# Kernel tuning notes

Measured on AMD Instinct MI355X. Metric: run time of the kernel, lower is better.

## Reference

```python
import jax, jax.numpy as jnp
import numpy as np

B = 2_000_000
L = 64
STEPS = 10
LAT_CONST = 5 * 0.03 / 200 + 0.06  # queue*lat/bw + 0.06
GRAD_CONST = 1.0 / 0.06
SEND_CONST = 2.0 / 3.0


def setup_inputs() -> dict:
    key = jax.random.key(0)
    ks = jax.random.split(key, 5)
    x = jax.random.normal(ks[0], (B, 7), dtype=jnp.float32)
    # column 0 is the loop counter i; program assumes it starts at 0 -> 10 iterations
    x = x.at[:, 0].set(0.0)
    W1 = jax.random.normal(ks[1], (3, L), dtype=jnp.float32) * 0.1
    b1 = jnp.zeros((L,), dtype=jnp.float32)
    W2 = jax.random.normal(ks[2], (L, L), dtype=jnp.float32) * 0.1
    b2 = jnp.zeros((L,), dtype=jnp.float32)
    W3 = jax.random.normal(ks[3], (L, 1), dtype=jnp.float32) * 0.1
    b3 = jnp.zeros((1,), dtype=jnp.float32)
    return {"x": x, "W1": W1, "b1": b1, "W2": W2, "b2": b2, "W3": W3, "b3": b3}


def _mlp(feat, W1, b1, W2, b2, W3, b3):
    h = jax.nn.relu(feat @ W1 + b1)
    h = jax.nn.relu(h @ W2 + b2)
    return jax.nn.sigmoid(h @ W3 + b3)[:, 0]


def reference(x, W1, b1, W2, b2, W3, b3):
    def step(state, _):
        x2 = state[:, 2]
        x6 = state[:, 6]
        # IfElse on column 6 vs comparison_bar=0.0:
        #   body  (x6 <= 0): x2 * (x6 + 1)          (assign_upper_sender_ratio)
        #   else  (x6 >  0): x2 * ((1 - x6) / 1)    (assign_down_sender_ratio, sub_l = left-sub)
        x2 = jnp.where(x6 <= 0.0, x2 * (x6 + 1.0), x2 * (1.0 - x6))
        x4 = x2 + LAT_CONST            # latency_ratio
        x5 = x2 * SEND_CONST           # sending_ratio
        x3 = x4 * GRAD_CONST           # latency_gradient
        feat = jnp.stack([x3, x4, x5], axis=1)  # [B,3]
        a = _mlp(feat, W1, b1, W2, b2, W3, b3)  # new action -> column 2
        new_state = state.at[:, 0].add(1.0)
        new_state = new_state.at[:, 2].set(a)
        new_state = new_state.at[:, 3].set(x3)
        new_state = new_state.at[:, 4].set(x4)
        new_state = new_state.at[:, 5].set(x5)
        return new_state, None

    final, _ = jax.lax.scan(step, x, None, length=STEPS)
    return final
```

## Files before the change

### kernel.cpp

```cpp
#include <hip/hip_runtime.h>
#include <math.h>

#define LAT_CONST  ((float)(5.0 * 0.03 / 200.0 + 0.06))
#define GRAD_CONST ((float)(1.0 / 0.06))
#define SEND_CONST ((float)(2.0 / 3.0))

#define NW   2048
#define LOW_ (-24.f)
#define HIW_ (24.f)
#define HW_  ((HIW_ - LOW_) / (float)NW)
#define IHW_ ((float)NW / (HIW_ - LOW_))
#define CW_  (-LOW_ * IHW_)
#define N2   2048
#define LO2  (-6.25f)
#define HI2  (1.25f)
#define H2   ((HI2 - LO2) / (float)N2)
#define IH2  ((float)N2 / (HI2 - LO2))
#define C2   (-LO2 * IH2)

#define GSZ   2080
#define GPCK  2064

__global__ __launch_bounds__(256)
void build_table_kernel(const float* __restrict__ W1, const float* __restrict__ b1,
                        const float* __restrict__ W2, const float* __restrict__ b2,
                        const float* __restrict__ W3, const float* __restrict__ b3,
                        float* __restrict__ g1, float* __restrict__ g2)
{
    __shared__ float pl[4][64];

    const int lane = threadIdx.x & 63;
    const int w    = threadIdx.x >> 6;
    const int i    = blockIdx.x * 64 + lane;

    float t;
    if (i < GSZ) t = LOW_ + (float)i * HW_;
    else         t = LO2 + (float)(i - GSZ) * H2;

    float x4 = t + LAT_CONST;
    float x5 = t * SEND_CONST;
    float x3 = x4 * GRAD_CONST;

    float h1v[64];
#pragma unroll
    for (int j = 0; j < 64; ++j) {
        float acc = b1[j];
        acc = fmaf(x3, W1[j],       acc);
        acc = fmaf(x4, W1[64 + j],  acc);
        acc = fmaf(x5, W1[128 + j], acc);
        h1v[j] = fmaxf(acc, 0.f);
    }

    const int j0 = w * 16;
    float acc[16];
#pragma unroll
    for (int u = 0; u < 16; ++u) acc[u] = b2[j0 + u];
#pragma unroll
    for (int k = 0; k < 64; ++k) {
        const float* __restrict__ w2r = W2 + k * 64 + j0;
#pragma unroll
        for (int u = 0; u < 16; ++u)
            acc[u] = fmaf(h1v[k], w2r[u], acc[u]);
    }
    float partial = 0.f;
#pragma unroll
    for (int u = 0; u < 16; ++u)
        partial = fmaf(fmaxf(acc[u], 0.f), W3[j0 + u], partial);

    pl[w][lane] = partial;
    __syncthreads();

    if (w == 0) {
        float logit = b3[0] + ((pl[0][lane] + pl[1][lane]) + (pl[2][lane] + pl[3][lane]));
        float g = 1.f / (1.f + expf(-logit));
        if (i < GSZ) g1[i] = g;
        else         g2[i - GSZ] = g;
    }
}

#define CHUNK 256
#define BLOCK 256
#define MAXGRID 1280

typedef unsigned int u32;
typedef __attribute__((address_space(3))) u32 lds_u32_t;
typedef __attribute__((address_space(1))) const u32 glb_u32_t;

__device__ __forceinline__ void gload16(const void* g, void* l) {
    __builtin_amdgcn_global_load_lds((glb_u32_t*)g, (lds_u32_t*)l, 16, 0, 0);
}

__device__ __forceinline__ u32 bfpack(float a, float b) {
    u32 ua = __float_as_uint(a), ub = __float_as_uint(b);
    ua = (ua + 0x7fffu + ((ua >> 16) & 1u)) >> 16;
    ub = (ub + 0x7fffu + ((ub >> 16) & 1u)) & 0xffff0000u;
    return (ua & 0xffffu) | ub;
}

__device__ __forceinline__ float lerp_pk(u32 u, float fr) {
    float e0 = __uint_as_float(u << 16);
    float e1 = __uint_as_float(u & 0xffff0000u);
    return fmaf(e1 - e0, fr, e0);
}

__global__ __launch_bounds__(BLOCK)
void rows_kernel(const float* __restrict__ x, const float* __restrict__ g1,
                 const float* __restrict__ g2, float* __restrict__ out,
                 int B, int nChunks)
{
    __shared__ u32 tw[GPCK];
    __shared__ u32 tn[GPCK];
    __shared__ __align__(16) float buf[2][CHUNK * 7];

    const int tid = threadIdx.x;
    const int c0  = blockIdx.x;

    {
        int rows0 = min(CHUNK, B - c0 * CHUNK);
        int nf40  = (rows0 * 7) >> 2;
        const float4* src = (const float4*)(x + (size_t)c0 * CHUNK * 7);
        for (int i = tid; i < nf40; i += BLOCK)
            gload16(src + i, &buf[0][i * 4]);
    }
    for (int i = tid; i < GPCK / 4; i += BLOCK) {
        float4 v = ((const float4*)g1)[i];
        float nx = g1[i * 4 + 4];
        tw[i*4+0] = bfpack(v.x, v.y); tw[i*4+1] = bfpack(v.y, v.z);
        tw[i*4+2] = bfpack(v.z, v.w); tw[i*4+3] = bfpack(v.w, nx);
        float4 q = ((const float4*)g2)[i];
        float ny = g2[i * 4 + 4];
        tn[i*4+0] = bfpack(q.x, q.y); tn[i*4+1] = bfpack(q.y, q.z);
        tn[i*4+2] = bfpack(q.z, q.w); tn[i*4+3] = bfpack(q.w, ny);
    }
    __syncthreads();

    int cur = 0;
    for (int c = c0; c < nChunks; c += gridDim.x) {
        int cn = c + gridDim.x;
        if (cn < nChunks) {
            int rowsN = min(CHUNK, B - cn * CHUNK);
            int nf4N  = (rowsN * 7) >> 2;
            const float4* src = (const float4*)(x + (size_t)cn * CHUNK * 7);
            for (int i = tid; i < nf4N; i += BLOCK)
                gload16(src + i, &buf[cur ^ 1][i * 4]);
        }

        int rows = min(CHUNK, B - c * CHUNK);
        float* bfr = buf[cur];
        for (int r = tid; r < rows; r += BLOCK) {
            float* row = bfr + r * 7;
            float x0 = row[0], x2 = row[2], x6 = row[6];
            float f = (x6 <= 0.f) ? (x6 + 1.f) : (1.f - x6);
            {
                float p = fmaf(x2, f * IHW_, CW_);
                p = fminf(fmaxf(p, 0.f), (float)NW);
                int idx = (int)p; float fr = p - (float)idx;
                x2 = lerp_pk(tw[idx], fr);
            }
            float af2 = f * IH2;
#pragma unroll
            for (int s = 0; s < 8; ++s) {
                float p = fmaf(x2, af2, C2);
                p = fminf(fmaxf(p, 0.f), (float)N2);
                int idx = (int)p; float fr = p - (float)idx;
                x2 = lerp_pk(tn[idx], fr);
            }
            float t = x2 * f;
            float p = fmaf(t, IH2, C2);
            p = fminf(fmaxf(p, 0.f), (float)N2);
            int idx = (int)p; float fr = p - (float)idx;
            float x2f = lerp_pk(tn[idx], fr);
            float x4 = t + LAT_CONST;
            row[0] = x0 + 10.f;
            row[2] = x2f;
            row[3] = x4 * GRAD_CONST;
            row[4] = x4;
            row[5] = t * SEND_CONST;
        }
        __syncthreads();

        {
            int nf4 = (rows * 7) >> 2;
            float4* dst = (float4*)(out + (size_t)c * CHUNK * 7);
            const float4* s4 = (const float4*)bfr;
            for (int i = tid; i < nf4; i += BLOCK) dst[i] = s4[i];
        }
        __syncthreads();
        cur ^= 1;
    }
}

static inline size_t align16h(size_t v) { return (v + 15) & ~(size_t)15; }

extern "C" void kernel_launch(void* const* d_in, const int* in_sizes, int n_in,
                              void* d_out, int out_size, void* d_ws, size_t ws_size,
                              hipStream_t stream)
{
    const float* x  = (const float*)d_in[0];
    const float* W1 = (const float*)d_in[1];
    const float* b1 = (const float*)d_in[2];
    const float* W2 = (const float*)d_in[3];
    const float* b2 = (const float*)d_in[4];
    const float* W3 = (const float*)d_in[5];
    const float* b3 = (const float*)d_in[6];
    float* out = (float*)d_out;

    int B = in_sizes[0] / 7;

    char* ws = (char*)d_ws;
    float* g1 = (float*)ws;
    float* g2 = (float*)(ws + align16h((size_t)GSZ * 4));

    int nChunks = (B + CHUNK - 1) / CHUNK;
    int grid    = (nChunks < MAXGRID) ? nChunks : MAXGRID;

    hipLaunchKernelGGL(build_table_kernel, dim3((2 * GSZ) / 64), dim3(256), 0, stream,
                       W1, b1, W2, b2, W3, b3, g1, g2);
    hipLaunchKernelGGL(rows_kernel, dim3(grid), dim3(BLOCK), 0, stream,
                       x, g1, g2, out, B, nChunks);
}
```

Before: 39.19 us.

## Drop first-step LDS table, use contiguous chunk ranges per block, raise grid

Removes the first-step bf16 table from LDS and reads that one lookup directly from global g1 in fp32. This halves per-block table LDS so more blocks fit per CU, and the grid cap rises from 1280 to 1792. Each block now handles a contiguous range of chunks instead of a grid stride, and tail handling for row counts not divisible by 4 floats is added. The cost is one scattered global gather per row for the first lookup.

```diff
diff --git a/kernel.cpp b/kernel.cpp
--- a/kernel.cpp
+++ b/kernel.cpp
@@ -80,7 +80,7 @@
 
 #define CHUNK 256
 #define BLOCK 256
-#define MAXGRID 1280
+#define MAXBLK 1792
 
 typedef unsigned int u32;
 typedef __attribute__((address_space(3))) u32 lds_u32_t;
@@ -88,6 +88,9 @@
 
 __device__ __forceinline__ void gload16(const void* g, void* l) {
     __builtin_amdgcn_global_load_lds((glb_u32_t*)g, (lds_u32_t*)l, 16, 0, 0);
+}
+__device__ __forceinline__ void gload4(const void* g, void* l) {
+    __builtin_amdgcn_global_load_lds((glb_u32_t*)g, (lds_u32_t*)l, 4, 0, 0);
 }
 
 __device__ __forceinline__ u32 bfpack(float a, float b) {
@@ -106,27 +109,27 @@
 __global__ __launch_bounds__(BLOCK)
 void rows_kernel(const float* __restrict__ x, const float* __restrict__ g1,
                  const float* __restrict__ g2, float* __restrict__ out,
-                 int B, int nChunks)
+                 int B, int nChunks, int grid)
 {
-    __shared__ u32 tw[GPCK];
     __shared__ u32 tn[GPCK];
     __shared__ __align__(16) float buf[2][CHUNK * 7];
 
     const int tid = threadIdx.x;
-    const int c0  = blockIdx.x;
+    const long long b = blockIdx.x;
+    const int cb = (int)(b * (long long)nChunks / grid);
+    const int ce = (int)((b + 1) * (long long)nChunks / grid);
 
     {
-        int rows0 = min(CHUNK, B - c0 * CHUNK);
-        int nf40  = (rows0 * 7) >> 2;
-        const float4* src = (const float4*)(x + (size_t)c0 * CHUNK * 7);
+        int rows0 = min(CHUNK, B - cb * CHUNK);
+        int nfl0  = rows0 * 7;
+        int nf40  = nfl0 >> 2;
+        const float* src = x + (size_t)cb * CHUNK * 7;
         for (int i = tid; i < nf40; i += BLOCK)
-            gload16(src + i, &buf[0][i * 4]);
+            gload16((const float4*)src + i, &buf[0][i * 4]);
+        for (int i = (nf40 << 2) + tid; i < nfl0; i += BLOCK)
+            gload4(src + i, &buf[0][i]);
     }
     for (int i = tid; i < GPCK / 4; i += BLOCK) {
-        float4 v = ((const float4*)g1)[i];
-        float nx = g1[i * 4 + 4];
-        tw[i*4+0] = bfpack(v.x, v.y); tw[i*4+1] = bfpack(v.y, v.z);
-        tw[i*4+2] = bfpack(v.z, v.w); tw[i*4+3] = bfpack(v.w, nx);
         float4 q = ((const float4*)g2)[i];
         float ny = g2[i * 4 + 4];
         tn[i*4+0] = bfpack(q.x, q.y); tn[i*4+1] = bfpack(q.y, q.z);
@@ -135,14 +138,16 @@
     __syncthreads();
 
     int cur = 0;
-    for (int c = c0; c < nChunks; c += gridDim.x) {
-        int cn = c + gridDim.x;
-        if (cn < nChunks) {
-            int rowsN = min(CHUNK, B - cn * CHUNK);
-            int nf4N  = (rowsN * 7) >> 2;
-            const float4* src = (const float4*)(x + (size_t)cn * CHUNK * 7);
+    for (int c = cb; c < ce; ++c) {
+        if (c + 1 < ce) {
+            int rowsN = min(CHUNK, B - (c + 1) * CHUNK);
+            int nflN  = rowsN * 7;
+            int nf4N  = nflN >> 2;
+            const float* src = x + (size_t)(c + 1) * CHUNK * 7;
             for (int i = tid; i < nf4N; i += BLOCK)
-                gload16(src + i, &buf[cur ^ 1][i * 4]);
+                gload16((const float4*)src + i, &buf[cur ^ 1][i * 4]);
+            for (int i = (nf4N << 2) + tid; i < nflN; i += BLOCK)
+                gload4(src + i, &buf[cur ^ 1][i]);
         }
 
         int rows = min(CHUNK, B - c * CHUNK);
@@ -155,7 +160,8 @@
                 float p = fmaf(x2, f * IHW_, CW_);
                 p = fminf(fmaxf(p, 0.f), (float)NW);
                 int idx = (int)p; float fr = p - (float)idx;
-                x2 = lerp_pk(tw[idx], fr);
+                float e0 = g1[idx], e1 = g1[idx + 1];
+                x2 = fmaf(e1 - e0, fr, e0);
             }
             float af2 = f * IH2;
 #pragma unroll
@@ -180,10 +186,12 @@
         __syncthreads();
 
         {
-            int nf4 = (rows * 7) >> 2;
-            float4* dst = (float4*)(out + (size_t)c * CHUNK * 7);
+            int nfl = rows * 7;
+            int nf4 = nfl >> 2;
+            float* dst = out + (size_t)c * CHUNK * 7;
             const float4* s4 = (const float4*)bfr;
-            for (int i = tid; i < nf4; i += BLOCK) dst[i] = s4[i];
+            for (int i = tid; i < nf4; i += BLOCK) ((float4*)dst)[i] = s4[i];
+            for (int i = (nf4 << 2) + tid; i < nfl; i += BLOCK) dst[i] = bfr[i];
         }
         __syncthreads();
         cur ^= 1;
@@ -212,10 +220,10 @@
     float* g2 = (float*)(ws + align16h((size_t)GSZ * 4));
 
     int nChunks = (B + CHUNK - 1) / CHUNK;
-    int grid    = (nChunks < MAXGRID) ? nChunks : MAXGRID;
+    int grid    = (nChunks < MAXBLK) ? nChunks : MAXBLK;
 
     hipLaunchKernelGGL(build_table_kernel, dim3((2 * GSZ) / 64), dim3(256), 0, stream,
                        W1, b1, W2, b2, W3, b3, g1, g2);
     hipLaunchKernelGGL(rows_kernel, dim3(grid), dim3(BLOCK), 0, stream,
-                       x, g1, g2, out, B, nChunks);
-}
+                       x, g1, g2, out, B, nChunks, grid);
+}
```

New measurement: 39.65 us. About the same (+1.2%).

## Process four rows per thread from registers instead of LDS-staged chunk loop

Applied to the files above, without the earlier changes.

Replaces the persistent grid-stride loop, which staged 256-row chunks into double-buffered LDS via global_load_lds, with a flat launch where each thread loads four rows (seven float4s) straight into registers and writes them back directly. The four rows' table-lookup chains are interleaved for instruction-level parallelism. The first-step lookup now reads the fp32 g1 table from global memory, so the bf16-packed tw LDS table and its per-block build are dropped. In exchange, more blocks are launched, each rebuilding the tn LDS table, and each thread's float4 accesses are strided across lanes, which may coalesce less well.

```diff
diff --git a/kernel.cpp b/kernel.cpp
--- a/kernel.cpp
+++ b/kernel.cpp
@@ -21,6 +21,8 @@
 #define GSZ   2080
 #define GPCK  2064
 
+typedef unsigned int u32;
+
 __global__ __launch_bounds__(256)
 void build_table_kernel(const float* __restrict__ W1, const float* __restrict__ b1,
                         const float* __restrict__ W2, const float* __restrict__ b2,
@@ -78,17 +80,7 @@
     }
 }
 
-#define CHUNK 256
 #define BLOCK 256
-#define MAXGRID 1280
-
-typedef unsigned int u32;
-typedef __attribute__((address_space(3))) u32 lds_u32_t;
-typedef __attribute__((address_space(1))) const u32 glb_u32_t;
-
-__device__ __forceinline__ void gload16(const void* g, void* l) {
-    __builtin_amdgcn_global_load_lds((glb_u32_t*)g, (lds_u32_t*)l, 16, 0, 0);
-}
 
 __device__ __forceinline__ u32 bfpack(float a, float b) {
     u32 ua = __float_as_uint(a), ub = __float_as_uint(b);
@@ -105,28 +97,12 @@
 
 __global__ __launch_bounds__(BLOCK)
 void rows_kernel(const float* __restrict__ x, const float* __restrict__ g1,
-                 const float* __restrict__ g2, float* __restrict__ out,
-                 int B, int nChunks)
+                 const float* __restrict__ g2, float* __restrict__ out, int B)
 {
-    __shared__ u32 tw[GPCK];
     __shared__ u32 tn[GPCK];
-    __shared__ __align__(16) float buf[2][CHUNK * 7];
 
     const int tid = threadIdx.x;
-    const int c0  = blockIdx.x;
-
-    {
-        int rows0 = min(CHUNK, B - c0 * CHUNK);
-        int nf40  = (rows0 * 7) >> 2;
-        const float4* src = (const float4*)(x + (size_t)c0 * CHUNK * 7);
-        for (int i = tid; i < nf40; i += BLOCK)
-            gload16(src + i, &buf[0][i * 4]);
-    }
     for (int i = tid; i < GPCK / 4; i += BLOCK) {
-        float4 v = ((const float4*)g1)[i];
-        float nx = g1[i * 4 + 4];
-        tw[i*4+0] = bfpack(v.x, v.y); tw[i*4+1] = bfpack(v.y, v.z);
-        tw[i*4+2] = bfpack(v.z, v.w); tw[i*4+3] = bfpack(v.w, nx);
         float4 q = ((const float4*)g2)[i];
         float ny = g2[i * 4 + 4];
         tn[i*4+0] = bfpack(q.x, q.y); tn[i*4+1] = bfpack(q.y, q.z);
@@ -134,31 +110,86 @@
     }
     __syncthreads();
 
-    int cur = 0;
-    for (int c = c0; c < nChunks; c += gridDim.x) {
-        int cn = c + gridDim.x;
-        if (cn < nChunks) {
-            int rowsN = min(CHUNK, B - cn * CHUNK);
-            int nf4N  = (rowsN * 7) >> 2;
-            const float4* src = (const float4*)(x + (size_t)cn * CHUNK * 7);
-            for (int i = tid; i < nf4N; i += BLOCK)
-                gload16(src + i, &buf[cur ^ 1][i * 4]);
-        }
-
-        int rows = min(CHUNK, B - c * CHUNK);
-        float* bfr = buf[cur];
-        for (int r = tid; r < rows; r += BLOCK) {
-            float* row = bfr + r * 7;
-            float x0 = row[0], x2 = row[2], x6 = row[6];
+    const long long gtid = (long long)blockIdx.x * BLOCK + tid;
+    const long long r0 = gtid * 4;
+    if (r0 >= B) return;
+
+    if (r0 + 4 <= B) {
+        const float4* __restrict__ src = (const float4*)(x + r0 * 7);
+        float fl[28];
+        {
+            float4 q;
+            q = src[0]; fl[0]=q.x; fl[1]=q.y; fl[2]=q.z; fl[3]=q.w;
+            q = src[1]; fl[4]=q.x; fl[5]=q.y; fl[6]=q.z; fl[7]=q.w;
+            q = src[2]; fl[8]=q.x; fl[9]=q.y; fl[10]=q.z; fl[11]=q.w;
+            q = src[3]; fl[12]=q.x; fl[13]=q.y; fl[14]=q.z; fl[15]=q.w;
+            q = src[4]; fl[16]=q.x; fl[17]=q.y; fl[18]=q.z; fl[19]=q.w;
+            q = src[5]; fl[20]=q.x; fl[21]=q.y; fl[22]=q.z; fl[23]=q.w;
+            q = src[6]; fl[24]=q.x; fl[25]=q.y; fl[26]=q.z; fl[27]=q.w;
+        }
+
+        float x2v[4], fv[4], af2[4];
+#pragma unroll
+        for (int k = 0; k < 4; ++k) {
+            float x6 = fl[7 * k + 6];
+            x2v[k] = fl[7 * k + 2];
+            fv[k]  = (x6 <= 0.f) ? (x6 + 1.f) : (1.f - x6);
+            af2[k] = fv[k] * IH2;
+        }
+#pragma unroll
+        for (int k = 0; k < 4; ++k) {
+            float p = fmaf(x2v[k], fv[k] * IHW_, CW_);
+            p = fminf(fmaxf(p, 0.f), (float)NW);
+            int idx = (int)p; float fr = p - (float)idx;
+            float e0 = g1[idx], e1 = g1[idx + 1];
+            x2v[k] = fmaf(e1 - e0, fr, e0);
+        }
+#pragma unroll
+        for (int s = 0; s < 8; ++s) {
+#pragma unroll
+            for (int k = 0; k < 4; ++k) {
+                float p = fmaf(x2v[k], af2[k], C2);
+                p = fminf(fmaxf(p, 0.f), (float)N2);
+                int idx = (int)p; float fr = p - (float)idx;
+                x2v[k] = lerp_pk(tn[idx], fr);
+            }
+        }
+#pragma unroll
+        for (int k = 0; k < 4; ++k) {
+            float t = x2v[k] * fv[k];
+            float p = fmaf(t, IH2, C2);
+            p = fminf(fmaxf(p, 0.f), (float)N2);
+            int idx = (int)p; float fr = p - (float)idx;
+            float x2f = lerp_pk(tn[idx], fr);
+            float x4 = t + LAT_CONST;
+            fl[7 * k + 0] += 10.f;
+            fl[7 * k + 2] = x2f;
+            fl[7 * k + 3] = x4 * GRAD_CONST;
+            fl[7 * k + 4] = x4;
+            fl[7 * k + 5] = t * SEND_CONST;
+        }
+
+        float4* __restrict__ dst = (float4*)(out + r0 * 7);
+        dst[0] = make_float4(fl[0],  fl[1],  fl[2],  fl[3]);
+        dst[1] = make_float4(fl[4],  fl[5],  fl[6],  fl[7]);
+        dst[2] = make_float4(fl[8],  fl[9],  fl[10], fl[11]);
+        dst[3] = make_float4(fl[12], fl[13], fl[14], fl[15]);
+        dst[4] = make_float4(fl[16], fl[17], fl[18], fl[19]);
+        dst[5] = make_float4(fl[20], fl[21], fl[22], fl[23]);
+        dst[6] = make_float4(fl[24], fl[25], fl[26], fl[27]);
+    } else {
+        for (long long r = r0; r < B; ++r) {
+            const float* row = x + r * 7;
+            float x0 = row[0], x1 = row[1], x2 = row[2], x6 = row[6];
             float f = (x6 <= 0.f) ? (x6 + 1.f) : (1.f - x6);
             {
                 float p = fmaf(x2, f * IHW_, CW_);
                 p = fminf(fmaxf(p, 0.f), (float)NW);
                 int idx = (int)p; float fr = p - (float)idx;
-                x2 = lerp_pk(tw[idx], fr);
+                float e0 = g1[idx], e1 = g1[idx + 1];
+                x2 = fmaf(e1 - e0, fr, e0);
             }
             float af2 = f * IH2;
-#pragma unroll
             for (int s = 0; s < 8; ++s) {
                 float p = fmaf(x2, af2, C2);
                 p = fminf(fmaxf(p, 0.f), (float)N2);
@@ -171,22 +202,15 @@
             int idx = (int)p; float fr = p - (float)idx;
             float x2f = lerp_pk(tn[idx], fr);
             float x4 = t + LAT_CONST;
-            row[0] = x0 + 10.f;
-            row[2] = x2f;
-            row[3] = x4 * GRAD_CONST;
-            row[4] = x4;
-            row[5] = t * SEND_CONST;
-        }
-        __syncthreads();
-
-        {
-            int nf4 = (rows * 7) >> 2;
-            float4* dst = (float4*)(out + (size_t)c * CHUNK * 7);
-            const float4* s4 = (const float4*)bfr;
-            for (int i = tid; i < nf4; i += BLOCK) dst[i] = s4[i];
-        }
-        __syncthreads();
-        cur ^= 1;
+            float* o = out + r * 7;
+            o[0] = x0 + 10.f;
+            o[1] = x1;
+            o[2] = x2f;
+            o[3] = x4 * GRAD_CONST;
+            o[4] = x4;
+            o[5] = t * SEND_CONST;
+            o[6] = x6;
+        }
     }
 }
 
@@ -211,11 +235,11 @@
     float* g1 = (float*)ws;
     float* g2 = (float*)(ws + align16h((size_t)GSZ * 4));
 
-    int nChunks = (B + CHUNK - 1) / CHUNK;
-    int grid    = (nChunks < MAXGRID) ? nChunks : MAXGRID;
+    long long nthreads = ((long long)B + 3) / 4;
+    int grid = (int)((nthreads + BLOCK - 1) / BLOCK);
 
     hipLaunchKernelGGL(build_table_kernel, dim3((2 * GSZ) / 64), dim3(256), 0, stream,
                        W1, b1, W2, b2, W3, b3, g1, g2);
     hipLaunchKernelGGL(rows_kernel, dim3(grid), dim3(BLOCK), 0, stream,
-                       x, g1, g2, out, B, nChunks);
-}
+                       x, g1, g2, out, B);
+}
```

Measured after the change: 52.61 us. 34.2% more time.

## Give each wavefront its own contiguous chunk range and LDS double buffer

Applied to the files above, without the earlier changes.

Replaces block-wide 256-row chunks, which needed two __syncthreads per iteration, with per-wave 64-row slabs. Each wavefront owns a contiguous range of slabs and double-buffers them through global_load_lds, using an explicit vmcnt wait instead of block barriers. The range is assigned by proportional split and any tail rows are handled directly from global memory by the last wave. This aims to remove barrier stalls and let waves progress independently, but it relies on the hand-written vmcnt count being correct and on stores not being included in that counter.

```diff
diff --git a/kernel.cpp b/kernel.cpp
--- a/kernel.cpp
+++ b/kernel.cpp
@@ -21,6 +21,8 @@
 #define GSZ   2080
 #define GPCK  2064
 
+typedef unsigned int u32;
+
 __global__ __launch_bounds__(256)
 void build_table_kernel(const float* __restrict__ W1, const float* __restrict__ b1,
                         const float* __restrict__ W2, const float* __restrict__ b2,
@@ -78,11 +80,10 @@
     }
 }
 
-#define CHUNK 256
 #define BLOCK 256
-#define MAXGRID 1280
-
-typedef unsigned int u32;
+#define WCH   64
+#define SLABF (WCH * 7)
+
 typedef __attribute__((address_space(3))) u32 lds_u32_t;
 typedef __attribute__((address_space(1))) const u32 glb_u32_t;
 
@@ -106,50 +107,89 @@
 __global__ __launch_bounds__(BLOCK)
 void rows_kernel(const float* __restrict__ x, const float* __restrict__ g1,
                  const float* __restrict__ g2, float* __restrict__ out,
-                 int B, int nChunks)
+                 int B, int nChunks, int nWaves)
 {
     __shared__ u32 tw[GPCK];
     __shared__ u32 tn[GPCK];
-    __shared__ __align__(16) float buf[2][CHUNK * 7];
-
-    const int tid = threadIdx.x;
-    const int c0  = blockIdx.x;
-
-    {
-        int rows0 = min(CHUNK, B - c0 * CHUNK);
-        int nf40  = (rows0 * 7) >> 2;
-        const float4* src = (const float4*)(x + (size_t)c0 * CHUNK * 7);
-        for (int i = tid; i < nf40; i += BLOCK)
-            gload16(src + i, &buf[0][i * 4]);
+    __shared__ __align__(16) float slab[4][2][SLABF];
+
+    const int tid  = threadIdx.x;
+    const int lane = tid & 63;
+    const int wid  = tid >> 6;
+    const long long gw = (long long)blockIdx.x * 4 + wid;
+    const int cb = (int)(gw * (long long)nChunks / nWaves);
+    const int ce = (int)((gw + 1) * (long long)nChunks / nWaves);
+
+    if (cb < ce) {
+        const float4* src4 = (const float4*)(x + (size_t)cb * SLABF);
+        float* d = slab[wid][0];
+        gload16(src4 + lane, d + lane * 4);
+        if (lane < 48) gload16(src4 + 64 + lane, d + (64 + lane) * 4);
     }
     for (int i = tid; i < GPCK / 4; i += BLOCK) {
-        float4 v = ((const float4*)g1)[i];
+        float4 q = ((const float4*)g1)[i];
         float nx = g1[i * 4 + 4];
-        tw[i*4+0] = bfpack(v.x, v.y); tw[i*4+1] = bfpack(v.y, v.z);
-        tw[i*4+2] = bfpack(v.z, v.w); tw[i*4+3] = bfpack(v.w, nx);
-        float4 q = ((const float4*)g2)[i];
+        tw[i*4+0] = bfpack(q.x, q.y); tw[i*4+1] = bfpack(q.y, q.z);
+        tw[i*4+2] = bfpack(q.z, q.w); tw[i*4+3] = bfpack(q.w, nx);
+        float4 r = ((const float4*)g2)[i];
         float ny = g2[i * 4 + 4];
-        tn[i*4+0] = bfpack(q.x, q.y); tn[i*4+1] = bfpack(q.y, q.z);
-        tn[i*4+2] = bfpack(q.z, q.w); tn[i*4+3] = bfpack(q.w, ny);
+        tn[i*4+0] = bfpack(r.x, r.y); tn[i*4+1] = bfpack(r.y, r.z);
+        tn[i*4+2] = bfpack(r.z, r.w); tn[i*4+3] = bfpack(r.w, ny);
     }
     __syncthreads();
 
     int cur = 0;
-    for (int c = c0; c < nChunks; c += gridDim.x) {
-        int cn = c + gridDim.x;
-        if (cn < nChunks) {
-            int rowsN = min(CHUNK, B - cn * CHUNK);
-            int nf4N  = (rowsN * 7) >> 2;
-            const float4* src = (const float4*)(x + (size_t)cn * CHUNK * 7);
-            for (int i = tid; i < nf4N; i += BLOCK)
-                gload16(src + i, &buf[cur ^ 1][i * 4]);
-        }
-
-        int rows = min(CHUNK, B - c * CHUNK);
-        float* bfr = buf[cur];
-        for (int r = tid; r < rows; r += BLOCK) {
-            float* row = bfr + r * 7;
-            float x0 = row[0], x2 = row[2], x6 = row[6];
+    for (int c = cb; c < ce; ++c) {
+        asm volatile("s_waitcnt vmcnt(2)" ::: "memory");
+        __builtin_amdgcn_sched_barrier(0);
+
+        if (c + 1 < ce) {
+            const float4* src4 = (const float4*)(x + (size_t)(c + 1) * SLABF);
+            float* d = slab[wid][cur ^ 1];
+            gload16(src4 + lane, d + lane * 4);
+            if (lane < 48) gload16(src4 + 64 + lane, d + (64 + lane) * 4);
+        }
+
+        float* row = slab[wid][cur] + lane * 7;
+        float x0 = row[0], x2 = row[2], x6 = row[6];
+        float f = (x6 <= 0.f) ? (x6 + 1.f) : (1.f - x6);
+        {
+            float p = fmaf(x2, f * IHW_, CW_);
+            p = fminf(fmaxf(p, 0.f), (float)NW);
+            int idx = (int)p; float fr = p - (float)idx;
+            x2 = lerp_pk(tw[idx], fr);
+        }
+        float af2 = f * IH2;
+#pragma unroll
+        for (int s = 0; s < 8; ++s) {
+            float p = fmaf(x2, af2, C2);
+            p = fminf(fmaxf(p, 0.f), (float)N2);
+            int idx = (int)p; float fr = p - (float)idx;
+            x2 = lerp_pk(tn[idx], fr);
+        }
+        float t = x2 * f;
+        float p = fmaf(t, IH2, C2);
+        p = fminf(fmaxf(p, 0.f), (float)N2);
+        int idx = (int)p; float fr = p - (float)idx;
+        float x2f = lerp_pk(tn[idx], fr);
+        float x4 = t + LAT_CONST;
+        row[0] = x0 + 10.f;
+        row[2] = x2f;
+        row[3] = x4 * GRAD_CONST;
+        row[4] = x4;
+        row[5] = t * SEND_CONST;
+
+        const float4* s4 = (const float4*)slab[wid][cur];
+        float4* dst = (float4*)(out + (size_t)c * SLABF);
+        dst[lane] = s4[lane];
+        if (lane < 48) dst[64 + lane] = s4[64 + lane];
+        cur ^= 1;
+    }
+
+    if (gw == (long long)nWaves - 1) {
+        for (long long r = (long long)nChunks * WCH + lane; r < B; r += 64) {
+            const float* rowg = x + r * 7;
+            float x0 = rowg[0], x1 = rowg[1], x2 = rowg[2], x6 = rowg[6];
             float f = (x6 <= 0.f) ? (x6 + 1.f) : (1.f - x6);
             {
                 float p = fmaf(x2, f * IHW_, CW_);
@@ -158,7 +198,6 @@
                 x2 = lerp_pk(tw[idx], fr);
             }
             float af2 = f * IH2;
-#pragma unroll
             for (int s = 0; s < 8; ++s) {
                 float p = fmaf(x2, af2, C2);
                 p = fminf(fmaxf(p, 0.f), (float)N2);
@@ -171,22 +210,15 @@
             int idx = (int)p; float fr = p - (float)idx;
             float x2f = lerp_pk(tn[idx], fr);
             float x4 = t + LAT_CONST;
-            row[0] = x0 + 10.f;
-            row[2] = x2f;
-            row[3] = x4 * GRAD_CONST;
-            row[4] = x4;
-            row[5] = t * SEND_CONST;
-        }
-        __syncthreads();
-
-        {
-            int nf4 = (rows * 7) >> 2;
-            float4* dst = (float4*)(out + (size_t)c * CHUNK * 7);
-            const float4* s4 = (const float4*)bfr;
-            for (int i = tid; i < nf4; i += BLOCK) dst[i] = s4[i];
-        }
-        __syncthreads();
-        cur ^= 1;
+            float* o = out + r * 7;
+            o[0] = x0 + 10.f;
+            o[1] = x1;
+            o[2] = x2f;
+            o[3] = x4 * GRAD_CONST;
+            o[4] = x4;
+            o[5] = t * SEND_CONST;
+            o[6] = x6;
+        }
     }
 }
 
@@ -211,11 +243,14 @@
     float* g1 = (float*)ws;
     float* g2 = (float*)(ws + align16h((size_t)GSZ * 4));
 
-    int nChunks = (B + CHUNK - 1) / CHUNK;
-    int grid    = (nChunks < MAXGRID) ? nChunks : MAXGRID;
+    int nChunks = B / WCH;
+    int grid = 1280;
+    int maxUseful = (nChunks + 3) / 4;
+    if (grid > maxUseful) grid = maxUseful > 0 ? maxUseful : 1;
+    int nWaves = grid * 4;
 
     hipLaunchKernelGGL(build_table_kernel, dim3((2 * GSZ) / 64), dim3(256), 0, stream,
                        W1, b1, W2, b2, W3, b3, g1, g2);
     hipLaunchKernelGGL(rows_kernel, dim3(grid), dim3(BLOCK), 0, stream,
-                       x, g1, g2, out, B, nChunks);
-}
+                       x, g1, g2, out, B, nChunks, nWaves);
+}
```

Result: slower. 40.85 us (+4.2%).
